# Optimization experiments

Hardware: AMD Instinct MI355X
Metric: run time of the kernel (lower is better)

The kernel has to match this reference:

```python
import jax, jax.numpy as jnp
import numpy as np

N_HEADS, D_MODEL, D_HEAD = 16, 1024, 64
BATCH, SEQ = 2, 2048
INIT_RANGE = 0.02


def setup_inputs() -> dict:
    key = jax.random.key(0)
    ks = jax.random.split(key, 5)
    x = jax.random.normal(ks[0], (BATCH, SEQ, D_MODEL), dtype=jnp.float32)
    W_Q = jax.random.normal(ks[1], (N_HEADS, D_MODEL, D_HEAD), dtype=jnp.float32) * INIT_RANGE
    W_K = jax.random.normal(ks[2], (N_HEADS, D_MODEL, D_HEAD), dtype=jnp.float32) * INIT_RANGE
    W_V = jax.random.normal(ks[3], (N_HEADS, D_MODEL, D_HEAD), dtype=jnp.float32) * INIT_RANGE
    W_O = jax.random.normal(ks[4], (N_HEADS, D_HEAD, D_MODEL), dtype=jnp.float32) * INIT_RANGE
    b_Q = jnp.zeros((N_HEADS, D_HEAD), dtype=jnp.float32)
    b_K = jnp.zeros((N_HEADS, D_HEAD), dtype=jnp.float32)
    b_V = jnp.zeros((N_HEADS, D_HEAD), dtype=jnp.float32)
    b_O = jnp.zeros((D_MODEL,), dtype=jnp.float32)
    return {"normalized_resid_pre": x, "W_Q": W_Q, "W_K": W_K, "W_V": W_V,
            "W_O": W_O, "b_Q": b_Q, "b_K": b_K, "b_V": b_V, "b_O": b_O}


def reference(normalized_resid_pre, W_Q, W_K, W_V, W_O, b_Q, b_K, b_V, b_O):
    x = normalized_resid_pre  # [b, s, d_model]
    q = jnp.einsum('bsm,hmd->bshd', x, W_Q) + b_Q  # [b, s, h, d_head]
    k = jnp.einsum('bsm,hmd->bshd', x, W_K) + b_K
    v = jnp.einsum('bsm,hmd->bshd', x, W_V) + b_V
    scores = jnp.einsum('bqhd,bkhd->bhqk', q, k) / jnp.sqrt(jnp.float32(D_HEAD))
    seq = x.shape[1]
    causal = jnp.tril(jnp.ones((seq, seq), dtype=bool))  # True where allowed
    scores = jnp.where(causal, scores, jnp.float32(-jnp.inf))
    pattern = jax.nn.softmax(scores, axis=-1)  # [b, h, q, k]
    z = jnp.einsum('bhqk,bkhd->bqhd', pattern, v)
    attn_out = jnp.einsum('bqhd,hdm->bqm', z, W_O) + b_O
    return attn_out
```

## Files before the change

kernel.cpp:

```cpp
#include <hip/hip_runtime.h>
#include <hip/hip_bf16.h>

#define BATCH 2
#define SEQL 2048
#define NH 16
#define DH 64
#define DM 1024
#define LDK 72

typedef __hip_bfloat16 bf16;
typedef __attribute__((ext_vector_type(8))) short  bf16x8;
typedef __attribute__((ext_vector_type(4))) float  f32x4;

__device__ __forceinline__ void gl_lds16(const void* g, void* l) {
    __builtin_amdgcn_global_load_lds(
        (const __attribute__((address_space(1))) unsigned int*)g,
        (__attribute__((address_space(3))) unsigned int*)l, 16, 0, 0);
}

__global__ __launch_bounds__(256) void xconv_kernel(
    const float* __restrict__ x, bf16* __restrict__ xb)
{
    const size_t i = ((size_t)blockIdx.x * 256 + threadIdx.x) * 4;
    const float4 v = *(const float4*)(x + i);
    bf16 o[4];
    o[0] = __float2bfloat16(v.x); o[1] = __float2bfloat16(v.y);
    o[2] = __float2bfloat16(v.z); o[3] = __float2bfloat16(v.w);
    *(uint2*)(xb + i) = *(const uint2*)o;
}

__global__ __launch_bounds__(256) void wtrans_kernel(
    const float* __restrict__ Wq, const float* __restrict__ Wk,
    const float* __restrict__ Wv, const float* __restrict__ Wo,
    bf16* __restrict__ Wt)
{
    __shared__ float ts[64][65];
    const int zi = blockIdx.z;
    const float* src = (zi == 0) ? Wq : (zi == 1) ? Wk : (zi == 2) ? Wv : Wo;
    bf16* dst = Wt + (size_t)zi * DM * DM;
    const int row0 = blockIdx.y * 64;
    const int col0 = blockIdx.x * 64;
    const int tx = threadIdx.x & 63;
    const int ty = threadIdx.x >> 6;

    if (zi < 3) {
        const int h = col0 >> 6;
        #pragma unroll
        for (int i = 0; i < 16; ++i) {
            const int r = ty + 4 * i;
            ts[r][tx] = src[h * (DM * DH) + (row0 + r) * DH + tx];
        }
    } else {
        #pragma unroll
        for (int i = 0; i < 16; ++i) {
            const int r = ty + 4 * i;
            ts[r][tx] = src[(size_t)(row0 + r) * DM + col0 + tx];
        }
    }
    __syncthreads();
    #pragma unroll
    for (int i = 0; i < 16; ++i) {
        const int rr = ty + 4 * i;
        dst[(size_t)(col0 + rr) * DM + row0 + tx] = __float2bfloat16(ts[tx][rr]);
    }
}

__global__ __launch_bounds__(256) void qkv_gemm(
    const bf16* __restrict__ xb, const bf16* __restrict__ Wt,
    const float* __restrict__ bq, const float* __restrict__ bk, const float* __restrict__ bv,
    bf16* __restrict__ qkv)
{
    __shared__ __align__(16) bf16 As[128 * 32];
    __shared__ __align__(16) bf16 Bs[128 * 32];

    const int t = threadIdx.x;
    const int lane = t & 63, w = t >> 6;
    const int ml = lane & 15, quad = lane >> 4;
    const int wr = w >> 1, wc = w & 1;
    const int bn = blockIdx.x, bm = blockIdx.y, which = blockIdx.z;

    const bf16* A0 = xb + (size_t)(bm * 128) * DM;
    const bf16* B0 = Wt + (size_t)which * DM * DM + (size_t)(bn * 128) * DM;
    const float* bias = (which == 0) ? bq : (which == 1) ? bk : bv;
    bf16* outb = qkv + (size_t)which * (BATCH * SEQL * NH * DH);

    f32x4 acc[4][4];
    #pragma unroll
    for (int i = 0; i < 4; ++i)
        #pragma unroll
        for (int j = 0; j < 4; ++j) acc[i][j] = (f32x4){0.f, 0.f, 0.f, 0.f};

    for (int kt = 0; kt < DM / 32; ++kt) {
        const int k0 = kt * 32;
        __syncthreads();
        #pragma unroll
        for (int j = 0; j < 2; ++j) {
            const int flat = t + j * 256;
            const int r = flat >> 2, c = (flat & 3) * 8;
            gl_lds16(A0 + (size_t)r * DM + k0 + c, &As[flat * 8]);
            gl_lds16(B0 + (size_t)r * DM + k0 + c, &Bs[flat * 8]);
        }
        __syncthreads();
        bf16x8 af[4], bfr[4];
        #pragma unroll
        for (int i = 0; i < 4; ++i)
            af[i] = *(const bf16x8*)&As[(wr * 64 + i * 16 + ml) * 32 + quad * 8];
        #pragma unroll
        for (int j = 0; j < 4; ++j)
            bfr[j] = *(const bf16x8*)&Bs[(wc * 64 + j * 16 + ml) * 32 + quad * 8];
        #pragma unroll
        for (int i = 0; i < 4; ++i)
            #pragma unroll
            for (int j = 0; j < 4; ++j)
                acc[i][j] = __builtin_amdgcn_mfma_f32_16x16x32_bf16(af[i], bfr[j], acc[i][j], 0, 0, 0);
    }

    float bb[4];
    #pragma unroll
    for (int j = 0; j < 4; ++j) bb[j] = bias[bn * 128 + wc * 64 + j * 16 + ml];

    #pragma unroll
    for (int i = 0; i < 4; ++i) {
        #pragma unroll
        for (int rg = 0; rg < 4; ++rg) {
            const int row = bm * 128 + wr * 64 + i * 16 + quad * 4 + rg;
            const int b = row >> 11;
            const int s = row & (SEQL - 1);
            #pragma unroll
            for (int j = 0; j < 4; ++j) {
                const int col = bn * 128 + wc * 64 + j * 16 + ml;
                const int h = col >> 6, d = col & 63;
                outb[(((size_t)(b * NH + h)) * SEQL + s) * DH + d] =
                    __float2bfloat16(acc[i][j][rg] + bb[j]);
            }
        }
    }
}

__global__ __launch_bounds__(256) void oproj_gemm(
    const bf16* __restrict__ zb, const bf16* __restrict__ Bt,
    const float* __restrict__ bo, float* __restrict__ out)
{
    __shared__ __align__(16) bf16 As[128 * 32];
    __shared__ __align__(16) bf16 Bs[128 * 32];

    const int t = threadIdx.x;
    const int lane = t & 63, w = t >> 6;
    const int ml = lane & 15, quad = lane >> 4;
    const int wr = w >> 1, wc = w & 1;
    const int bn = blockIdx.x, bm = blockIdx.y;

    const bf16* A0 = zb + (size_t)(bm * 128) * DM;
    const bf16* B0 = Bt + (size_t)(bn * 128) * DM;

    f32x4 acc[4][4];
    #pragma unroll
    for (int i = 0; i < 4; ++i)
        #pragma unroll
        for (int j = 0; j < 4; ++j) acc[i][j] = (f32x4){0.f, 0.f, 0.f, 0.f};

    for (int kt = 0; kt < DM / 32; ++kt) {
        const int k0 = kt * 32;
        __syncthreads();
        #pragma unroll
        for (int j = 0; j < 2; ++j) {
            const int flat = t + j * 256;
            const int r = flat >> 2, c = (flat & 3) * 8;
            gl_lds16(A0 + (size_t)r * DM + k0 + c, &As[flat * 8]);
            gl_lds16(B0 + (size_t)r * DM + k0 + c, &Bs[flat * 8]);
        }
        __syncthreads();
        bf16x8 af[4], bfr[4];
        #pragma unroll
        for (int i = 0; i < 4; ++i)
            af[i] = *(const bf16x8*)&As[(wr * 64 + i * 16 + ml) * 32 + quad * 8];
        #pragma unroll
        for (int j = 0; j < 4; ++j)
            bfr[j] = *(const bf16x8*)&Bs[(wc * 64 + j * 16 + ml) * 32 + quad * 8];
        #pragma unroll
        for (int i = 0; i < 4; ++i)
            #pragma unroll
            for (int j = 0; j < 4; ++j)
                acc[i][j] = __builtin_amdgcn_mfma_f32_16x16x32_bf16(af[i], bfr[j], acc[i][j], 0, 0, 0);
    }

    float bb[4];
    #pragma unroll
    for (int j = 0; j < 4; ++j) bb[j] = bo[bn * 128 + wc * 64 + j * 16 + ml];

    #pragma unroll
    for (int i = 0; i < 4; ++i) {
        #pragma unroll
        for (int rg = 0; rg < 4; ++rg) {
            const int row = bm * 128 + wr * 64 + i * 16 + quad * 4 + rg;
            #pragma unroll
            for (int j = 0; j < 4; ++j) {
                const int col = bn * 128 + wc * 64 + j * 16 + ml;
                out[(size_t)row * DM + col] = acc[i][j][rg] + bb[j];
            }
        }
    }
}

__global__ __launch_bounds__(256) void attn_kernel(
    const bf16* __restrict__ qg, const bf16* __restrict__ kg, const bf16* __restrict__ vg,
    bf16* __restrict__ z)
{
    __shared__ bf16     KsS[64 * LDK];
    __shared__ unsigned VtS[64 * 32];
    __shared__ bf16     PsS[4][16 * LDK];

    const int t    = threadIdx.x;
    const int lane = t & 63;
    const int w    = t >> 6;
    const int m    = lane & 15;
    const int quad = lane >> 4;

    const int bh = blockIdx.x;
    const int b  = bh >> 4;
    const int h  = bh & 15;
    const int qt = (gridDim.y - 1) - blockIdx.y;
    const int q0 = qt * 64;

    const size_t base = (size_t)bh * SEQL * DH;

    const int rp = t >> 3;
    const int a8 = t & 7;
    const int d0 = a8 * 8;

    bf16x8 aq[2];
    {
        const bf16* qp = qg + base + (size_t)(q0 + w * 16 + m) * DH + quad * 8;
        aq[0] = *(const bf16x8*)(qp);
        aq[1] = *(const bf16x8*)(qp + 32);
    }

    f32x4 zacc[4];
    #pragma unroll
    for (int nt = 0; nt < 4; ++nt) zacc[nt] = (f32x4){0.f, 0.f, 0.f, 0.f};
    float m_i[4] = {-1e30f, -1e30f, -1e30f, -1e30f};
    float l_i[4] = {0.f, 0.f, 0.f, 0.f};

    bf16* Psw = PsS[w];

    for (int kt = 0; kt <= qt; ++kt) {
        __syncthreads();
        {
            const bf16* kr = kg + base + (size_t)(kt * 64 + 2 * rp) * DH + d0;
            const bf16* vr = vg + base + (size_t)(kt * 64 + 2 * rp) * DH + d0;
            const uint4 k0 = *(const uint4*)(kr);
            const uint4 k1 = *(const uint4*)(kr + DH);
            const uint4 v0 = *(const uint4*)(vr);
            const uint4 v1 = *(const uint4*)(vr + DH);
            *(uint4*)(&KsS[(2 * rp) * LDK + d0])     = k0;
            *(uint4*)(&KsS[(2 * rp + 1) * LDK + d0]) = k1;
            const unsigned short* h0 = (const unsigned short*)&v0;
            const unsigned short* h1 = (const unsigned short*)&v1;
            #pragma unroll
            for (int j = 0; j < 8; ++j) {
                const unsigned pw = (unsigned)h0[j] | ((unsigned)h1[j] << 16);
                VtS[(d0 + j) * 32 + (rp ^ ((j ^ a8) << 2))] = pw;
            }
        }
        __syncthreads();

        f32x4 sc[4];
        #pragma unroll
        for (int nt = 0; nt < 4; ++nt) sc[nt] = (f32x4){0.f, 0.f, 0.f, 0.f};
        #pragma unroll
        for (int ks = 0; ks < 2; ++ks) {
            #pragma unroll
            for (int nt = 0; nt < 4; ++nt) {
                const bf16x8 bk = *(const bf16x8*)(&KsS[(nt * 16 + m) * LDK + ks * 32 + quad * 8]);
                sc[nt] = __builtin_amdgcn_mfma_f32_16x16x32_bf16(aq[ks], bk, sc[nt], 0, 0, 0);
            }
        }
        #pragma unroll
        for (int nt = 0; nt < 4; ++nt)
            #pragma unroll
            for (int rg = 0; rg < 4; ++rg) sc[nt][rg] *= 0.125f;
        if (kt == qt) {
            #pragma unroll
            for (int nt = 0; nt < 4; ++nt) {
                const int col = nt * 16 + m;
                #pragma unroll
                for (int rg = 0; rg < 4; ++rg) {
                    const int row = w * 16 + quad * 4 + rg;
                    if (col > row) sc[nt][rg] = -1e30f;
                }
            }
        }

        #pragma unroll
        for (int rg = 0; rg < 4; ++rg) {
            float mx = fmaxf(fmaxf(sc[0][rg], sc[1][rg]), fmaxf(sc[2][rg], sc[3][rg]));
            mx = fmaxf(mx, __shfl_xor(mx, 1));
            mx = fmaxf(mx, __shfl_xor(mx, 2));
            mx = fmaxf(mx, __shfl_xor(mx, 4));
            mx = fmaxf(mx, __shfl_xor(mx, 8));
            const float mn = fmaxf(m_i[rg], mx);
            const float al = __expf(m_i[rg] - mn);
            m_i[rg] = mn;
            float rs = 0.f;
            #pragma unroll
            for (int nt = 0; nt < 4; ++nt) {
                const float p = __expf(sc[nt][rg] - mn);
                Psw[(quad * 4 + rg) * LDK + nt * 16 + m] = __float2bfloat16(p);
                rs += p;
            }
            rs += __shfl_xor(rs, 1);
            rs += __shfl_xor(rs, 2);
            rs += __shfl_xor(rs, 4);
            rs += __shfl_xor(rs, 8);
            l_i[rg] = l_i[rg] * al + rs;
            #pragma unroll
            for (int nt = 0; nt < 4; ++nt) zacc[nt][rg] *= al;
        }

        #pragma unroll
        for (int ks = 0; ks < 2; ++ks) {
            const bf16x8 ap = *(const bf16x8*)(&Psw[m * LDK + ks * 32 + quad * 8]);
            #pragma unroll
            for (int nt = 0; nt < 4; ++nt) {
                const int n  = nt * 16 + m;
                const int p0 = ks * 16 + quad * 4;
                const int sw = ((n & 7) ^ ((n >> 3) & 7)) << 2;
                const bf16x8 bv = *(const bf16x8*)(&VtS[n * 32 + (p0 ^ sw)]);
                zacc[nt] = __builtin_amdgcn_mfma_f32_16x16x32_bf16(ap, bv, zacc[nt], 0, 0, 0);
            }
        }
    }

    float invl[4];
    #pragma unroll
    for (int rg = 0; rg < 4; ++rg) invl[rg] = 1.f / l_i[rg];
    #pragma unroll
    for (int nt = 0; nt < 4; ++nt) {
        const int d = nt * 16 + m;
        #pragma unroll
        for (int rg = 0; rg < 4; ++rg) {
            const int qrow = q0 + w * 16 + quad * 4 + rg;
            z[(((size_t)b * SEQL + qrow) * NH + h) * DH + d] =
                __float2bfloat16(zacc[nt][rg] * invl[rg]);
        }
    }
}

extern "C" void kernel_launch(void* const* d_in, const int* in_sizes, int n_in,
                              void* d_out, int out_size, void* d_ws, size_t ws_size,
                              hipStream_t stream)
{
    const float* x  = (const float*)d_in[0];
    const float* Wq = (const float*)d_in[1];
    const float* Wk = (const float*)d_in[2];
    const float* Wv = (const float*)d_in[3];
    const float* Wo = (const float*)d_in[4];
    const float* bq = (const float*)d_in[5];
    const float* bk = (const float*)d_in[6];
    const float* bv = (const float*)d_in[7];
    const float* bo = (const float*)d_in[8];
    float* out = (float*)d_out;

    const size_t TOK = (size_t)BATCH * SEQL;
    const size_t QKV = TOK * DM;
    bf16* xb  = (bf16*)d_ws;
    bf16* Wt  = xb + QKV;
    bf16* qkv = Wt + 4 * (size_t)DM * DM;
    bf16* zb  = qkv + 3 * QKV;

    xconv_kernel<<<dim3(TOK * DM / 1024), 256, 0, stream>>>(x, xb);
    wtrans_kernel<<<dim3(16, 16, 4), 256, 0, stream>>>(Wq, Wk, Wv, Wo, Wt);
    qkv_gemm<<<dim3(8, 32, 3), 256, 0, stream>>>(xb, Wt, bq, bk, bv, qkv);
    attn_kernel<<<dim3(BATCH * NH, SEQL / 64), 256, 0, stream>>>(
        qkv, qkv + QKV, qkv + 2 * QKV, zb);
    oproj_gemm<<<dim3(8, 32), 256, 0, stream>>>(zb, Wt + 3 * (size_t)DM * DM, bo, out);
}
```

Measured before the change: 210.2 us.

## Double attention query tile per block and fold softmax scale into Q projection

Each attention block now covers 128 query rows, with each wave owning two 16-row tiles, so every K/V tile staged in shared memory is reused by twice as many MFMAs and the grid is halved. The 1/sqrt(d)*log2(e) factor is folded into the Q projection epilogue, so the attention kernel drops its per-score multiply and uses exp2 directly. The cost is more registers per wave, a larger P buffer in LDS, and less parallelism (512 blocks). Causal masking now compares global row and column indices on the last two key tiles.

```diff
diff --git a/kernel.cpp b/kernel.cpp
--- a/kernel.cpp
+++ b/kernel.cpp
@@ -7,6 +7,8 @@
 #define DH 64
 #define DM 1024
 #define LDK 72
+#define LDP 80
+#define QSCALE 0.1803368801111244f
 
 typedef __hip_bfloat16 bf16;
 typedef __attribute__((ext_vector_type(8))) short  bf16x8;
@@ -83,6 +85,7 @@
     const bf16* B0 = Wt + (size_t)which * DM * DM + (size_t)(bn * 128) * DM;
     const float* bias = (which == 0) ? bq : (which == 1) ? bk : bv;
     bf16* outb = qkv + (size_t)which * (BATCH * SEQL * NH * DH);
+    const float oscale = (which == 0) ? QSCALE : 1.0f;
 
     f32x4 acc[4][4];
     #pragma unroll
@@ -131,7 +134,7 @@
                 const int col = bn * 128 + wc * 64 + j * 16 + ml;
                 const int h = col >> 6, d = col & 63;
                 outb[(((size_t)(b * NH + h)) * SEQL + s) * DH + d] =
-                    __float2bfloat16(acc[i][j][rg] + bb[j]);
+                    __float2bfloat16((acc[i][j][rg] + bb[j]) * oscale);
             }
         }
     }
@@ -208,7 +211,7 @@
 {
     __shared__ bf16     KsS[64 * LDK];
     __shared__ unsigned VtS[64 * 32];
-    __shared__ bf16     PsS[4][16 * LDK];
+    __shared__ bf16     PsS[4][32 * LDP];
 
     const int t    = threadIdx.x;
     const int lane = t & 63;
@@ -220,7 +223,7 @@
     const int b  = bh >> 4;
     const int h  = bh & 15;
     const int qt = (gridDim.y - 1) - blockIdx.y;
-    const int q0 = qt * 64;
+    const int q0 = qt * 128;
 
     const size_t base = (size_t)bh * SEQL * DH;
 
@@ -228,22 +231,29 @@
     const int a8 = t & 7;
     const int d0 = a8 * 8;
 
-    bf16x8 aq[2];
-    {
-        const bf16* qp = qg + base + (size_t)(q0 + w * 16 + m) * DH + quad * 8;
-        aq[0] = *(const bf16x8*)(qp);
-        aq[1] = *(const bf16x8*)(qp + 32);
-    }
-
-    f32x4 zacc[4];
-    #pragma unroll
-    for (int nt = 0; nt < 4; ++nt) zacc[nt] = (f32x4){0.f, 0.f, 0.f, 0.f};
-    float m_i[4] = {-1e30f, -1e30f, -1e30f, -1e30f};
-    float l_i[4] = {0.f, 0.f, 0.f, 0.f};
+    bf16x8 aq[2][2];
+    #pragma unroll
+    for (int rt = 0; rt < 2; ++rt) {
+        const bf16* qp = qg + base + (size_t)(q0 + w * 32 + rt * 16 + m) * DH + quad * 8;
+        aq[rt][0] = *(const bf16x8*)(qp);
+        aq[rt][1] = *(const bf16x8*)(qp + 32);
+    }
+
+    f32x4 zacc[2][4];
+    float m_i[2][4], l_i[2][4];
+    #pragma unroll
+    for (int rt = 0; rt < 2; ++rt)
+        #pragma unroll
+        for (int nt = 0; nt < 4; ++nt) zacc[rt][nt] = (f32x4){0.f, 0.f, 0.f, 0.f};
+    #pragma unroll
+    for (int rt = 0; rt < 2; ++rt)
+        #pragma unroll
+        for (int rg = 0; rg < 4; ++rg) { m_i[rt][rg] = -1e30f; l_i[rt][rg] = 0.f; }
 
     bf16* Psw = PsS[w];
-
-    for (int kt = 0; kt <= qt; ++kt) {
+    const int ktmax = 2 * qt + 1;
+
+    for (int kt = 0; kt <= ktmax; ++kt) {
         __syncthreads();
         {
             const bf16* kr = kg + base + (size_t)(kt * 64 + 2 * rp) * DH + d0;
@@ -264,84 +274,105 @@
         }
         __syncthreads();
 
-        f32x4 sc[4];
-        #pragma unroll
-        for (int nt = 0; nt < 4; ++nt) sc[nt] = (f32x4){0.f, 0.f, 0.f, 0.f};
+        f32x4 sc[2][4];
+        #pragma unroll
+        for (int rt = 0; rt < 2; ++rt)
+            #pragma unroll
+            for (int nt = 0; nt < 4; ++nt) sc[rt][nt] = (f32x4){0.f, 0.f, 0.f, 0.f};
         #pragma unroll
         for (int ks = 0; ks < 2; ++ks) {
-            #pragma unroll
-            for (int nt = 0; nt < 4; ++nt) {
-                const bf16x8 bk = *(const bf16x8*)(&KsS[(nt * 16 + m) * LDK + ks * 32 + quad * 8]);
-                sc[nt] = __builtin_amdgcn_mfma_f32_16x16x32_bf16(aq[ks], bk, sc[nt], 0, 0, 0);
-            }
-        }
-        #pragma unroll
-        for (int nt = 0; nt < 4; ++nt)
-            #pragma unroll
-            for (int rg = 0; rg < 4; ++rg) sc[nt][rg] *= 0.125f;
-        if (kt == qt) {
-            #pragma unroll
-            for (int nt = 0; nt < 4; ++nt) {
-                const int col = nt * 16 + m;
+            bf16x8 bk[4];
+            #pragma unroll
+            for (int nt = 0; nt < 4; ++nt)
+                bk[nt] = *(const bf16x8*)(&KsS[(nt * 16 + m) * LDK + ks * 32 + quad * 8]);
+            #pragma unroll
+            for (int rt = 0; rt < 2; ++rt)
                 #pragma unroll
-                for (int rg = 0; rg < 4; ++rg) {
-                    const int row = w * 16 + quad * 4 + rg;
-                    if (col > row) sc[nt][rg] = -1e30f;
+                for (int nt = 0; nt < 4; ++nt)
+                    sc[rt][nt] = __builtin_amdgcn_mfma_f32_16x16x32_bf16(aq[rt][ks], bk[nt], sc[rt][nt], 0, 0, 0);
+        }
+
+        if (kt >= 2 * qt) {
+            #pragma unroll
+            for (int rt = 0; rt < 2; ++rt) {
+                #pragma unroll
+                for (int nt = 0; nt < 4; ++nt) {
+                    const int colg = kt * 64 + nt * 16 + m;
+                    #pragma unroll
+                    for (int rg = 0; rg < 4; ++rg) {
+                        const int rowg = q0 + w * 32 + rt * 16 + quad * 4 + rg;
+                        if (colg > rowg) sc[rt][nt][rg] = -1e30f;
+                    }
                 }
             }
         }
 
         #pragma unroll
-        for (int rg = 0; rg < 4; ++rg) {
-            float mx = fmaxf(fmaxf(sc[0][rg], sc[1][rg]), fmaxf(sc[2][rg], sc[3][rg]));
-            mx = fmaxf(mx, __shfl_xor(mx, 1));
-            mx = fmaxf(mx, __shfl_xor(mx, 2));
-            mx = fmaxf(mx, __shfl_xor(mx, 4));
-            mx = fmaxf(mx, __shfl_xor(mx, 8));
-            const float mn = fmaxf(m_i[rg], mx);
-            const float al = __expf(m_i[rg] - mn);
-            m_i[rg] = mn;
-            float rs = 0.f;
-            #pragma unroll
-            for (int nt = 0; nt < 4; ++nt) {
-                const float p = __expf(sc[nt][rg] - mn);
-                Psw[(quad * 4 + rg) * LDK + nt * 16 + m] = __float2bfloat16(p);
-                rs += p;
-            }
-            rs += __shfl_xor(rs, 1);
-            rs += __shfl_xor(rs, 2);
-            rs += __shfl_xor(rs, 4);
-            rs += __shfl_xor(rs, 8);
-            l_i[rg] = l_i[rg] * al + rs;
-            #pragma unroll
-            for (int nt = 0; nt < 4; ++nt) zacc[nt][rg] *= al;
+        for (int rt = 0; rt < 2; ++rt) {
+            #pragma unroll
+            for (int rg = 0; rg < 4; ++rg) {
+                float mx = fmaxf(fmaxf(sc[rt][0][rg], sc[rt][1][rg]),
+                                 fmaxf(sc[rt][2][rg], sc[rt][3][rg]));
+                mx = fmaxf(mx, __shfl_xor(mx, 1));
+                mx = fmaxf(mx, __shfl_xor(mx, 2));
+                mx = fmaxf(mx, __shfl_xor(mx, 4));
+                mx = fmaxf(mx, __shfl_xor(mx, 8));
+                const float mn = fmaxf(m_i[rt][rg], mx);
+                const float al = __builtin_exp2f(m_i[rt][rg] - mn);
+                m_i[rt][rg] = mn;
+                float rs = 0.f;
+                #pragma unroll
+                for (int nt = 0; nt < 4; ++nt) {
+                    const float p = __builtin_exp2f(sc[rt][nt][rg] - mn);
+                    Psw[(rt * 16 + quad * 4 + rg) * LDP + nt * 16 + m] = __float2bfloat16(p);
+                    rs += p;
+                }
+                rs += __shfl_xor(rs, 1);
+                rs += __shfl_xor(rs, 2);
+                rs += __shfl_xor(rs, 4);
+                rs += __shfl_xor(rs, 8);
+                l_i[rt][rg] = l_i[rt][rg] * al + rs;
+                #pragma unroll
+                for (int nt = 0; nt < 4; ++nt) zacc[rt][nt][rg] *= al;
+            }
         }
 
         #pragma unroll
         for (int ks = 0; ks < 2; ++ks) {
-            const bf16x8 ap = *(const bf16x8*)(&Psw[m * LDK + ks * 32 + quad * 8]);
+            bf16x8 bv[4];
             #pragma unroll
             for (int nt = 0; nt < 4; ++nt) {
                 const int n  = nt * 16 + m;
                 const int p0 = ks * 16 + quad * 4;
                 const int sw = ((n & 7) ^ ((n >> 3) & 7)) << 2;
-                const bf16x8 bv = *(const bf16x8*)(&VtS[n * 32 + (p0 ^ sw)]);
-                zacc[nt] = __builtin_amdgcn_mfma_f32_16x16x32_bf16(ap, bv, zacc[nt], 0, 0, 0);
-            }
-        }
-    }
-
-    float invl[4];
-    #pragma unroll
-    for (int rg = 0; rg < 4; ++rg) invl[rg] = 1.f / l_i[rg];
-    #pragma unroll
-    for (int nt = 0; nt < 4; ++nt) {
-        const int d = nt * 16 + m;
-        #pragma unroll
-        for (int rg = 0; rg < 4; ++rg) {
-            const int qrow = q0 + w * 16 + quad * 4 + rg;
-            z[(((size_t)b * SEQL + qrow) * NH + h) * DH + d] =
-                __float2bfloat16(zacc[nt][rg] * invl[rg]);
+                bv[nt] = *(const bf16x8*)(&VtS[n * 32 + (p0 ^ sw)]);
+            }
+            bf16x8 ap[2];
+            #pragma unroll
+            for (int rt = 0; rt < 2; ++rt)
+                ap[rt] = *(const bf16x8*)(&Psw[(rt * 16 + m) * LDP + ks * 32 + quad * 8]);
+            #pragma unroll
+            for (int rt = 0; rt < 2; ++rt)
+                #pragma unroll
+                for (int nt = 0; nt < 4; ++nt)
+                    zacc[rt][nt] = __builtin_amdgcn_mfma_f32_16x16x32_bf16(ap[rt], bv[nt], zacc[rt][nt], 0, 0, 0);
+        }
+    }
+
+    #pragma unroll
+    for (int rt = 0; rt < 2; ++rt) {
+        float invl[4];
+        #pragma unroll
+        for (int rg = 0; rg < 4; ++rg) invl[rg] = 1.f / l_i[rt][rg];
+        #pragma unroll
+        for (int nt = 0; nt < 4; ++nt) {
+            const int d = nt * 16 + m;
+            #pragma unroll
+            for (int rg = 0; rg < 4; ++rg) {
+                const int qrow = q0 + w * 32 + rt * 16 + quad * 4 + rg;
+                z[(((size_t)b * SEQL + qrow) * NH + h) * DH + d] =
+                    __float2bfloat16(zacc[rt][nt][rg] * invl[rg]);
+            }
         }
     }
 }
@@ -371,7 +402,7 @@
     xconv_kernel<<<dim3(TOK * DM / 1024), 256, 0, stream>>>(x, xb);
     wtrans_kernel<<<dim3(16, 16, 4), 256, 0, stream>>>(Wq, Wk, Wv, Wo, Wt);
     qkv_gemm<<<dim3(8, 32, 3), 256, 0, stream>>>(xb, Wt, bq, bk, bv, qkv);
-    attn_kernel<<<dim3(BATCH * NH, SEQL / 64), 256, 0, stream>>>(
+    attn_kernel<<<dim3(BATCH * NH, SEQL / 128), 256, 0, stream>>>(
         qkv, qkv + QKV, qkv + 2 * QKV, zb);
     oproj_gemm<<<dim3(8, 32), 256, 0, stream>>>(zb, Wt + 3 * (size_t)DM * DM, bo, out);
 }
```

New measurement: 245.4 us. 16.7% more time.
